# Kernel tuning notes

Hardware: AMD Instinct MI355X
Metric: run time of the kernel (lower is better)

Reference implementation:

```python
import jax, jax.numpy as jnp
import numpy as np

N, E, H, NF, EF = 50000, 400000, 128, 10, 10


def setup_inputs() -> dict:
    key = jax.random.key(0)
    ks = iter(jax.random.split(key, 24))
    rn = lambda shape, s=0.1: jax.random.normal(next(ks), shape, jnp.float32) * s
    z = lambda shape: jnp.zeros(shape, jnp.float32)
    o = lambda shape: jnp.ones(shape, jnp.float32)
    return {
        "x": jax.random.normal(next(ks), (N, NF), jnp.float32),
        "edge_index": jax.random.randint(next(ks), (2, E), 0, N, jnp.int32),
        "edge_attr": jax.random.normal(next(ks), (E, EF), jnp.float32),
        "ne_w": rn((NF, H)), "ne_b": z(H), "ne_g": o(H), "ne_beta": z(H),
        "ee_w": rn((EF, H)), "ee_b": z(H), "ee_g": o(H), "ee_beta": z(H),
        "gate_w": rn((3 * H, H)), "gate_b": z(H),
        "gatA_w": rn((2, H, H)), "gatA_asrc": rn((2, 8, 16)), "gatA_adst": rn((2, 8, 16)), "gatA_bias": z((2, H)),
        "gatB_w": rn((H, H)), "gatB_asrc": rn((1, H)), "gatB_adst": rn((1, H)), "gatB_bias": z(H),
        "ln_g": o((3, H)), "ln_b": z((3, H)),
        "c1_w": rn((2 * H, H)), "c1_b": z(H), "cl1_g": o(H), "cl1_b": z(H),
        "c2_w": rn((H, H // 2)), "c2_b": z(H // 2), "cl2_g": o(H // 2), "cl2_b": z(H // 2),
        "c3_w": rn((H // 2, 2)), "c3_b": z(2),
    }


def _ln(x, g, b):
    m = x.mean(-1, keepdims=True)
    v = ((x - m) ** 2).mean(-1, keepdims=True)
    return (x - m) / jnp.sqrt(v + 1e-5) * g + b


def _gat(h, src, dst, n, w, asrc, adst, bias, concat):
    # PyG GATConv: lin (no bias), per-edge leaky_relu score, segment softmax over dst, scatter-add
    heads, dout = asrc.shape
    xp = (h @ w).reshape(n, heads, dout)             # [N, heads, dout]
    a_s = (xp * asrc).sum(-1)                        # [N, heads]
    a_d = (xp * adst).sum(-1)
    e = jax.nn.leaky_relu(a_s[src] + a_d[dst], 0.2)  # [E2, heads]
    m = jax.ops.segment_max(e, dst, num_segments=n)
    ex = jnp.exp(e - m[dst])
    s = jax.ops.segment_sum(ex, dst, num_segments=n)
    alpha = ex / s[dst]                               # [E2, heads]
    out = jax.ops.segment_sum(xp[src] * alpha[..., None], dst, num_segments=n)  # [N, heads, dout]
    out = out.reshape(n, heads * dout) if concat else out.mean(1)
    return out + bias


def reference(x, edge_index, edge_attr, ne_w, ne_b, ne_g, ne_beta, ee_w, ee_b, ee_g, ee_beta,
              gate_w, gate_b, gatA_w, gatA_asrc, gatA_adst, gatA_bias, gatB_w, gatB_asrc,
              gatB_adst, gatB_bias, ln_g, ln_b, c1_w, c1_b, cl1_g, cl1_b, c2_w, c2_b,
              cl2_g, cl2_b, c3_w, c3_b):
    n = x.shape[0]
    row, col = edge_index[0], edge_index[1]
    loops = jnp.arange(n, dtype=edge_index.dtype)     # GATConv add_self_loops=True
    src_sl = jnp.concatenate([row, loops])
    dst_sl = jnp.concatenate([col, loops])

    h = jax.nn.relu(_ln(x @ ne_w + ne_b, ne_g, ne_beta))      # node encoder (dropout=eval)
    for l in range(2):
        h = _gat(h, src_sl, dst_sl, n, gatA_w[l], gatA_asrc[l], gatA_adst[l], gatA_bias[l], True)
        h = jax.nn.relu(_ln(h, ln_g[l], ln_b[l]))
    h = _gat(h, src_sl, dst_sl, n, gatB_w, gatB_asrc, gatB_adst, gatB_bias, False)
    h = jax.nn.relu(_ln(h, ln_g[2], ln_b[2]))

    s = h[row]
    d = h[col]
    e = jax.nn.relu(_ln(edge_attr @ ee_w + ee_b, ee_g, ee_beta))  # edge encoder
    gate = jax.nn.sigmoid(jnp.concatenate([s, d, e], axis=1) @ gate_w + gate_b)
    s = s + gate * e
    d = d + gate * e

    zc = jax.nn.relu(_ln(jnp.concatenate([s, d], axis=1) @ c1_w + c1_b, cl1_g, cl1_b))
    zc = jax.nn.relu(_ln(zc @ c2_w + c2_b, cl2_g, cl2_b))
    return zc @ c3_w + c3_b                                   # [E, num_classes]
```

## Files before the change

kernel.cpp:

```cpp
#include <hip/hip_runtime.h>
#include <hip/hip_bf16.h>

#define H 128
#define NFEAT 10
#define EFEAT 10
#define XPS 144

typedef __attribute__((ext_vector_type(8))) short bf16x8;
typedef __attribute__((ext_vector_type(4))) float f32x4;

__device__ __forceinline__ float bflo(unsigned v) { return __uint_as_float(v << 16); }
__device__ __forceinline__ float bfhi(unsigned v) { return __uint_as_float(v & 0xffff0000u); }
__device__ __forceinline__ unsigned bfpack(float a, float b) {
    __hip_bfloat16 h0 = __float2bfloat16(a), h1 = __float2bfloat16(b);
    return (unsigned)(*(unsigned short*)&h0) | ((unsigned)(*(unsigned short*)&h1) << 16);
}

__global__ __launch_bounds__(256) void k_degree(const int* __restrict__ col,
                                                int* __restrict__ deg, int E, int N) {
    int i = blockIdx.x * blockDim.x + threadIdx.x;
    int E2 = E + N;
    if (i < E2) {
        int d = (i < E) ? col[i] : (i - E);
        atomicAdd(&deg[d], 1);
    }
}

__global__ __launch_bounds__(1024) void k_scan(const int* __restrict__ deg,
                                               int* __restrict__ offs,
                                               int* __restrict__ cursor, int N) {
    __shared__ int ps[1024];
    int t = threadIdx.x;
    int chunk = (N + 1023) / 1024;
    int begin = t * chunk;
    int end = begin + chunk; if (end > N) end = N;
    int s = 0;
    for (int i = begin; i < end; i++) s += deg[i];
    if (begin >= N) s = 0;
    ps[t] = s;
    __syncthreads();
    for (int off = 1; off < 1024; off <<= 1) {
        int v = (t >= off) ? ps[t - off] : 0;
        __syncthreads();
        ps[t] += v;
        __syncthreads();
    }
    int run = (t == 0) ? 0 : ps[t - 1];
    if (begin < N) {
        for (int i = begin; i < end; i++) {
            offs[i] = run;
            cursor[i] = run;
            run += deg[i];
        }
    }
    if (t == 1023) offs[N] = ps[1023];
}

__global__ __launch_bounds__(256) void k_scatter(const int* __restrict__ rowp,
                                                 const int* __restrict__ colp,
                                                 int* __restrict__ cursor,
                                                 int* __restrict__ srcs, int E, int N) {
    int i = blockIdx.x * blockDim.x + threadIdx.x;
    if (i < E + N) {
        int s, d;
        if (i < E) { s = rowp[i]; d = colp[i]; }
        else       { s = i - E;  d = i - E; }
        int pos = atomicAdd(&cursor[d], 1);
        srcs[pos] = s;
    }
}

__global__ __launch_bounds__(256) void k_node_enc(const float* __restrict__ x,
                                                  const float* __restrict__ wm,
                                                  const float* __restrict__ b,
                                                  const float* __restrict__ g,
                                                  const float* __restrict__ beta,
                                                  __hip_bfloat16* __restrict__ h, int N) {
    int t = threadIdx.x;
    int w = t >> 6, l = t & 63;
    int n = blockIdx.x * 4 + w;
    if (n >= N) return;
    float xs[NFEAT];
#pragma unroll
    for (int k = 0; k < NFEAT; k++) xs[k] = x[(size_t)n * NFEAT + k];
    float a0 = b[2 * l], a1 = b[2 * l + 1];
#pragma unroll
    for (int k = 0; k < NFEAT; k++) {
        float2 wv = *(const float2*)&wm[k * H + 2 * l];
        a0 += xs[k] * wv.x;
        a1 += xs[k] * wv.y;
    }
    float p = a0 + a1;
#pragma unroll
    for (int s = 1; s < 64; s <<= 1) p += __shfl_xor(p, s, 64);
    float mean = p * (1.0f / H);
    float d0 = a0 - mean, d1 = a1 - mean;
    float q = d0 * d0 + d1 * d1;
#pragma unroll
    for (int s = 1; s < 64; s <<= 1) q += __shfl_xor(q, s, 64);
    float rstd = rsqrtf(q * (1.0f / H) + 1e-5f);
    float y0 = fmaxf(d0 * rstd * g[2 * l] + beta[2 * l], 0.0f);
    float y1 = fmaxf(d1 * rstd * g[2 * l + 1] + beta[2 * l + 1], 0.0f);
    *(unsigned*)&h[(size_t)n * H + 2 * l] = bfpack(y0, y1);
}

__global__ __launch_bounds__(256, 2) void k_gat_xp_mfma(
        const __hip_bfloat16* __restrict__ h_bf,
        const __hip_bfloat16* __restrict__ wT,
        const float* __restrict__ asrc,
        const float* __restrict__ adst,
        __hip_bfloat16* __restrict__ xp_bf,
        float* __restrict__ a_d,
        int heads, int N) {
    __shared__ __hip_bfloat16 Ws[128 * 136];
    __shared__ __hip_bfloat16 As[64 * 136];
    int t = threadIdx.x;
    int n0 = blockIdx.x * 64;

#pragma unroll
    for (int it = 0; it < 2; it++) {
        int idx = it * 256 + t;
        int row = idx >> 2, seg = idx & 3;
        const uint4* src = (const uint4*)(wT + row * 128 + seg * 32);
        uint4 v0 = src[0], v1 = src[1], v2 = src[2], v3 = src[3];
        uint4* dst = (uint4*)&Ws[row * 136 + seg * 32];
        dst[0] = v0; dst[1] = v1; dst[2] = v2; dst[3] = v3;
    }
    {
        int row = t >> 2, seg = t & 3;
        int n = n0 + row; if (n >= N) n = N - 1;
        const uint4* src = (const uint4*)(h_bf + (size_t)n * 128 + seg * 32);
        uint4 v0 = src[0], v1 = src[1], v2 = src[2], v3 = src[3];
        uint4* dst = (uint4*)&As[row * 136 + seg * 32];
        dst[0] = v0; dst[1] = v1; dst[2] = v2; dst[3] = v3;
    }
    __syncthreads();

    int w = t >> 6, l = t & 63, ln15 = l & 15, quad = l >> 4, q8 = quad * 8;
    f32x4 acc[8] = {};
#pragma unroll
    for (int k = 0; k < 128; k += 32) {
        bf16x8 af = *(const bf16x8*)&As[(w * 16 + ln15) * 136 + k + q8];
#pragma unroll
        for (int i = 0; i < 8; i++) {
            bf16x8 bfr = *(const bf16x8*)&Ws[(i * 16 + ln15) * 136 + k + q8];
            acc[i] = __builtin_amdgcn_mfma_f32_16x16x32_bf16(af, bfr, acc[i], 0, 0, 0);
        }
    }

    if (heads == 8) {
#pragma unroll
        for (int i = 0; i < 8; i++) {
            float av = asrc[i * 16 + ln15], dvv = adst[i * 16 + ln15];
            float ps[4], pd[4];
#pragma unroll
            for (int r = 0; r < 4; r++) { ps[r] = acc[i][r] * av; pd[r] = acc[i][r] * dvv; }
#pragma unroll
            for (int s = 1; s < 16; s <<= 1) {
#pragma unroll
                for (int r = 0; r < 4; r++) {
                    ps[r] += __shfl_xor(ps[r], s, 64);
                    pd[r] += __shfl_xor(pd[r], s, 64);
                }
            }
            if (ln15 == 0) {
#pragma unroll
                for (int r = 0; r < 4; r++) {
                    int n = n0 + w * 16 + quad * 4 + r;
                    if (n < N) {
                        *(float*)&xp_bf[(size_t)n * XPS + 128 + 2 * i] = ps[r];
                        a_d[(size_t)n * 8 + i] = pd[r];
                    }
                }
            }
        }
    } else {
        float ps[4] = {0, 0, 0, 0}, pd[4] = {0, 0, 0, 0};
#pragma unroll
        for (int i = 0; i < 8; i++) {
            float av = asrc[i * 16 + ln15], dvv = adst[i * 16 + ln15];
#pragma unroll
            for (int r = 0; r < 4; r++) { ps[r] += acc[i][r] * av; pd[r] += acc[i][r] * dvv; }
        }
#pragma unroll
        for (int s = 1; s < 16; s <<= 1) {
#pragma unroll
            for (int r = 0; r < 4; r++) {
                ps[r] += __shfl_xor(ps[r], s, 64);
                pd[r] += __shfl_xor(pd[r], s, 64);
            }
        }
        if (ln15 == 0) {
#pragma unroll
            for (int r = 0; r < 4; r++) {
                int n = n0 + w * 16 + quad * 4 + r;
                if (n < N) {
                    *(float*)&xp_bf[(size_t)n * XPS + 128] = ps[r];
                    a_d[n] = pd[r];
                }
            }
        }
    }

#pragma unroll
    for (int i = 0; i < 8; i++) {
#pragma unroll
        for (int r = 0; r < 4; r++) {
            int n = n0 + w * 16 + quad * 4 + r;
            if (n < N) xp_bf[(size_t)n * XPS + i * 16 + ln15] = __float2bfloat16(acc[i][r]);
        }
    }
}

__global__ __launch_bounds__(256) void k_gat_agg(const __hip_bfloat16* __restrict__ xp,
                                                 const float* __restrict__ a_d,
                                                 const int* __restrict__ offs,
                                                 const int* __restrict__ srcs,
                                                 const float* __restrict__ bias,
                                                 const float* __restrict__ g,
                                                 const float* __restrict__ b,
                                                 __hip_bfloat16* __restrict__ hout,
                                                 int heads, int N) {
    int t = threadIdx.x;
    int w = t >> 6, l = t & 63;
    int n = blockIdx.x * 4 + w;
    if (n >= N) return;
    int head = (heads == 8) ? (l >> 3) : 0;
    float adv = a_d[(size_t)n * heads + head];
    int s0 = offs[n], s1 = offs[n + 1];
    float acc0 = 0.0f, acc1 = 0.0f, den = 0.0f;
    int j = s0;
    for (; j + 4 <= s1; j += 4) {
        int s_[4];
#pragma unroll
        for (int u = 0; u < 4; u++) s_[u] = srcs[j + u];
        float e_[4]; unsigned v_[4];
#pragma unroll
        for (int u = 0; u < 4; u++) {
            const __hip_bfloat16* xr = xp + (size_t)s_[u] * XPS;
            e_[u] = ((const float*)xr)[64 + head];
            v_[u] = *(const unsigned*)&xr[2 * l];
        }
#pragma unroll
        for (int u = 0; u < 4; u++) {
            float e = e_[u] + adv;
            e = (e >= 0.0f) ? e : 0.2f * e;
            float ex = __expf(e);
            den += ex;
            acc0 += ex * bflo(v_[u]);
            acc1 += ex * bfhi(v_[u]);
        }
    }
    for (; j < s1; j++) {
        int s = srcs[j];
        const __hip_bfloat16* xr = xp + (size_t)s * XPS;
        float e = ((const float*)xr)[64 + head] + adv;
        e = (e >= 0.0f) ? e : 0.2f * e;
        float ex = __expf(e);
        den += ex;
        unsigned v = *(const unsigned*)&xr[2 * l];
        acc0 += ex * bflo(v);
        acc1 += ex * bfhi(v);
    }
    float inv = 1.0f / den;
    float v0 = acc0 * inv + bias[2 * l];
    float v1 = acc1 * inv + bias[2 * l + 1];
    float p = v0 + v1;
#pragma unroll
    for (int s = 1; s < 64; s <<= 1) p += __shfl_xor(p, s, 64);
    float mean = p * (1.0f / H);
    float d0 = v0 - mean, d1 = v1 - mean;
    float q = d0 * d0 + d1 * d1;
#pragma unroll
    for (int s = 1; s < 64; s <<= 1) q += __shfl_xor(q, s, 64);
    float rstd = rsqrtf(q * (1.0f / H) + 1e-5f);
    float y0 = fmaxf(d0 * rstd * g[2 * l] + b[2 * l], 0.0f);
    float y1 = fmaxf(d1 * rstd * g[2 * l + 1] + b[2 * l + 1], 0.0f);
    *(unsigned*)&hout[(size_t)n * H + 2 * l] = bfpack(y0, y1);
}

__global__ __launch_bounds__(256) void k_wprep(const float* __restrict__ gate_w,
                                               const float* __restrict__ c1_w,
                                               const float* __restrict__ c2_w,
                                               const float* __restrict__ gatA_w,
                                               const float* __restrict__ gatB_w,
                                               const float* __restrict__ ee_w,
                                               __hip_bfloat16* __restrict__ gate_sw,
                                               __hip_bfloat16* __restrict__ c1_sw,
                                               __hip_bfloat16* __restrict__ c2_sw,
                                               __hip_bfloat16* __restrict__ wT3,
                                               __hip_bfloat16* __restrict__ ee_sw) {
    int i = blockIdx.x * blockDim.x + threadIdx.x;
    if (i < 49152) {
        int j = i & 7, lane = (i >> 3) & 63, rest = i >> 9;
        int nt = rest & 7, kc = rest >> 3;
        int n = nt * 16 + (lane & 15);
        int k = kc * 32 + (lane >> 4) * 8 + j;
        gate_sw[i] = __float2bfloat16(gate_w[k * 128 + n]);
    } else if (i < 81920) {
        int m = i - 49152;
        int j = m & 7, lane = (m >> 3) & 63, rest = m >> 9;
        int nt = rest & 7, kc = rest >> 3;
        int n = nt * 16 + (lane & 15);
        int k = kc * 32 + (lane >> 4) * 8 + j;
        c1_sw[m] = __float2bfloat16(c1_w[k * 128 + n]);
    } else if (i < 90112) {
        int m = i - 81920;
        int j = m & 7, lane = (m >> 3) & 63, rest = m >> 9;
        int nt = rest & 3, kc = rest >> 2;
        int n = nt * 16 + (lane & 15);
        int k = kc * 32 + (lane >> 4) * 8 + j;
        c2_sw[m] = __float2bfloat16(c2_w[k * 64 + n]);
    } else if (i < 139264) {
        int m = i - 90112;
        int mat = m / 16384, r = m % 16384;
        int n = r / 128, k = r % 128;
        const float* src = (mat < 2) ? (gatA_w + (size_t)mat * 16384) : gatB_w;
        wT3[m] = __float2bfloat16(src[k * 128 + n]);
    } else if (i < 143360) {
        int m = i - 139264;
        int j = m & 7, lane = (m >> 3) & 63, nt = (m >> 9) & 7;
        int n = nt * 16 + (lane & 15);
        int k = (lane >> 4) * 8 + j;
        ee_sw[m] = (k < EFEAT) ? __float2bfloat16(ee_w[k * 128 + n]) : __float2bfloat16(0.0f);
    }
}

__global__ __launch_bounds__(256, 4) void k_edge_cls_mfma(
        const __hip_bfloat16* __restrict__ h_bf,
        const int* __restrict__ rowp, const int* __restrict__ colp,
        const float* __restrict__ eattr,
        const __hip_bfloat16* __restrict__ ee_sw, const float* __restrict__ ee_b,
        const float* __restrict__ ee_g, const float* __restrict__ ee_beta,
        const __hip_bfloat16* __restrict__ gate_sw, const float* __restrict__ gate_b,
        const __hip_bfloat16* __restrict__ c1_sw, const float* __restrict__ c1_b,
        const float* __restrict__ cl1_g, const float* __restrict__ cl1_b,
        const __hip_bfloat16* __restrict__ c2_sw, const float* __restrict__ c2_b,
        const float* __restrict__ cl2_g, const float* __restrict__ cl2_b,
        const float* __restrict__ c3_w, const float* __restrict__ c3_b,
        float* __restrict__ out, int E) {
    __shared__ __align__(16) __hip_bfloat16 Bs[4 * 16 * 264];
    int t = threadIdx.x;
    int w = t >> 6, l = t & 63;
    int ln15 = l & 15, quad = l >> 4, q8 = quad * 8;
    int e0 = blockIdx.x * 64;
    int rbase = w * 16;
    __hip_bfloat16* B = Bs + w * (16 * 264);

    int eF = e0 + rbase + ln15; if (eF >= E) eF = E - 1;
    const __hip_bfloat16* rowS = h_bf + (size_t)rowp[eF] * 128;
    const __hip_bfloat16* rowD = h_bf + (size_t)colp[eF] * 128;

    {
        bf16x8 afe;
#pragma unroll
        for (int j = 0; j < 8; j++) {
            int k = q8 + j;
            float v = (k < EFEAT) ? eattr[(size_t)eF * EFEAT + k] : 0.0f;
            __hip_bfloat16 hv = __float2bfloat16(v);
            afe[j] = *(short*)&hv;
        }
        f32x4 acc[8] = {};
#pragma unroll
        for (int i = 0; i < 8; i++) {
            bf16x8 bfr = *(const bf16x8*)(ee_sw + ((size_t)i * 64 + l) * 8);
            acc[i] = __builtin_amdgcn_mfma_f32_16x16x32_bf16(afe, bfr, acc[i], 0, 0, 0);
        }
#pragma unroll
        for (int i = 0; i < 8; i++) {
            float cb = ee_b[i * 16 + ln15];
#pragma unroll
            for (int r = 0; r < 4; r++) acc[i][r] += cb;
        }
        float mean[4], rstd[4];
#pragma unroll
        for (int r = 0; r < 4; r++) {
            float p = 0.0f;
#pragma unroll
            for (int i = 0; i < 8; i++) p += acc[i][r];
            p += __shfl_xor(p, 1, 64); p += __shfl_xor(p, 2, 64);
            p += __shfl_xor(p, 4, 64); p += __shfl_xor(p, 8, 64);
            mean[r] = p * (1.0f / 128.0f);
        }
#pragma unroll
        for (int r = 0; r < 4; r++) {
            float q = 0.0f;
#pragma unroll
            for (int i = 0; i < 8; i++) { float d = acc[i][r] - mean[r]; q += d * d; }
            q += __shfl_xor(q, 1, 64); q += __shfl_xor(q, 2, 64);
            q += __shfl_xor(q, 4, 64); q += __shfl_xor(q, 8, 64);
            rstd[r] = rsqrtf(q * (1.0f / 128.0f) + 1e-5f);
        }
#pragma unroll
        for (int i = 0; i < 8; i++) {
            int cn = i * 16 + ln15;
            float g1 = ee_g[cn], b1 = ee_beta[cn];
#pragma unroll
            for (int r = 0; r < 4; r++) {
                int qr = quad * 4 + r;
                float y = fmaxf((acc[i][r] - mean[r]) * rstd[r] * g1 + b1, 0.0f);
                B[qr * 264 + cn] = __float2bfloat16(y);
            }
        }
    }

    {
        f32x4 acc[8] = {};
        bf16x8 fifo[4];
#pragma unroll
        for (int s = 0; s < 4; s++)
            fifo[s] = *(const bf16x8*)(gate_sw + ((size_t)s * 64 + l) * 8);
        bf16x8 acur = *(const bf16x8*)(rowS + q8);
        bf16x8 anx;
#pragma unroll
        for (int s = 0; s < 96; s++) {
            int kc = s >> 3, i = s & 7;
            if (i == 0 && kc < 11) {
                int k1 = kc + 1;
                if (k1 < 4)      anx = *(const bf16x8*)(rowS + k1 * 32 + q8);
                else if (k1 < 8) anx = *(const bf16x8*)(rowD + (k1 - 4) * 32 + q8);
                else             anx = *(const bf16x8*)&B[ln15 * 264 + (k1 - 8) * 32 + q8];
            }
            bf16x8 bcur = fifo[s & 3];
            if (s + 4 < 96)
                fifo[s & 3] = *(const bf16x8*)(gate_sw + ((size_t)(s + 4) * 64 + l) * 8);
            acc[i] = __builtin_amdgcn_mfma_f32_16x16x32_bf16(acur, bcur, acc[i], 0, 0, 0);
            if (i == 7) acur = anx;
        }
#pragma unroll
        for (int r = 0; r < 4; r++) {
            int qr = quad * 4 + r;
            int er = e0 + rbase + qr; if (er >= E) er = E - 1;
            const __hip_bfloat16* rS = h_bf + (size_t)rowp[er] * 128;
            const __hip_bfloat16* rD = h_bf + (size_t)colp[er] * 128;
#pragma unroll
            for (int i = 0; i < 8; i++) {
                int cn = i * 16 + ln15;
                float gt = 1.0f / (1.0f + __expf(-(acc[i][r] + gate_b[cn])));
                float ef = __bfloat162float(B[qr * 264 + cn]);
                float s  = __bfloat162float(rS[cn]);
                float d  = __bfloat162float(rD[cn]);
                B[qr * 264 + cn]       = __float2bfloat16(s + gt * ef);
                B[qr * 264 + 128 + cn] = __float2bfloat16(d + gt * ef);
            }
        }
    }

    {
        f32x4 acc[8] = {};
        bf16x8 fifo[4];
#pragma unroll
        for (int s = 0; s < 4; s++)
            fifo[s] = *(const bf16x8*)(c1_sw + ((size_t)s * 64 + l) * 8);
        bf16x8 acur = *(const bf16x8*)&B[ln15 * 264 + q8];
        bf16x8 anx;
#pragma unroll
        for (int s = 0; s < 64; s++) {
            int kc = s >> 3, i = s & 7;
            if (i == 0 && kc < 7)
                anx = *(const bf16x8*)&B[ln15 * 264 + (kc + 1) * 32 + q8];
            bf16x8 bcur = fifo[s & 3];
            if (s + 4 < 64)
                fifo[s & 3] = *(const bf16x8*)(c1_sw + ((size_t)(s + 4) * 64 + l) * 8);
            acc[i] = __builtin_amdgcn_mfma_f32_16x16x32_bf16(acur, bcur, acc[i], 0, 0, 0);
            if (i == 7) acur = anx;
        }
#pragma unroll
        for (int i = 0; i < 8; i++) {
            float cb = c1_b[i * 16 + ln15];
#pragma unroll
            for (int r = 0; r < 4; r++) acc[i][r] += cb;
        }
        float mean[4], rstd[4];
#pragma unroll
        for (int r = 0; r < 4; r++) {
            float p = 0.0f;
#pragma unroll
            for (int i = 0; i < 8; i++) p += acc[i][r];
            p += __shfl_xor(p, 1, 64); p += __shfl_xor(p, 2, 64);
            p += __shfl_xor(p, 4, 64); p += __shfl_xor(p, 8, 64);
            mean[r] = p * (1.0f / 128.0f);
        }
#pragma unroll
        for (int r = 0; r < 4; r++) {
            float q = 0.0f;
#pragma unroll
            for (int i = 0; i < 8; i++) { float d = acc[i][r] - mean[r]; q += d * d; }
            q += __shfl_xor(q, 1, 64); q += __shfl_xor(q, 2, 64);
            q += __shfl_xor(q, 4, 64); q += __shfl_xor(q, 8, 64);
            rstd[r] = rsqrtf(q * (1.0f / 128.0f) + 1e-5f);
        }
#pragma unroll
        for (int i = 0; i < 8; i++) {
            int cn = i * 16 + ln15;
            float g1 = cl1_g[cn], b1 = cl1_b[cn];
#pragma unroll
            for (int r = 0; r < 4; r++) {
                int qr = quad * 4 + r;
                float y = fmaxf((acc[i][r] - mean[r]) * rstd[r] * g1 + b1, 0.0f);
                B[qr * 264 + cn] = __float2bfloat16(y);
            }
        }
    }

    {
        f32x4 acc[4] = {};
        bf16x8 fifo[4];
#pragma unroll
        for (int s = 0; s < 4; s++)
            fifo[s] = *(const bf16x8*)(c2_sw + ((size_t)s * 64 + l) * 8);
        bf16x8 acur = *(const bf16x8*)&B[ln15 * 264 + q8];
        bf16x8 anx;
#pragma unroll
        for (int s = 0; s < 16; s++) {
            int kc = s >> 2, i = s & 3;
            if (i == 0 && kc < 3)
                anx = *(const bf16x8*)&B[ln15 * 264 + (kc + 1) * 32 + q8];
            bf16x8 bcur = fifo[s & 3];
            if (s + 4 < 16)
                fifo[s & 3] = *(const bf16x8*)(c2_sw + ((size_t)(s + 4) * 64 + l) * 8);
            acc[i] = __builtin_amdgcn_mfma_f32_16x16x32_bf16(acur, bcur, acc[i], 0, 0, 0);
            if (i == 3) acur = anx;
        }
#pragma unroll
        for (int i = 0; i < 4; i++) {
            float cb = c2_b[i * 16 + ln15];
#pragma unroll
            for (int r = 0; r < 4; r++) acc[i][r] += cb;
        }
        float mean[4], rstd[4];
#pragma unroll
        for (int r = 0; r < 4; r++) {
            float p = 0.0f;
#pragma unroll
            for (int i = 0; i < 4; i++) p += acc[i][r];
            p += __shfl_xor(p, 1, 64); p += __shfl_xor(p, 2, 64);
            p += __shfl_xor(p, 4, 64); p += __shfl_xor(p, 8, 64);
            mean[r] = p * (1.0f / 64.0f);
        }
#pragma unroll
        for (int r = 0; r < 4; r++) {
            float q = 0.0f;
#pragma unroll
            for (int i = 0; i < 4; i++) { float d = acc[i][r] - mean[r]; q += d * d; }
            q += __shfl_xor(q, 1, 64); q += __shfl_xor(q, 2, 64);
            q += __shfl_xor(q, 4, 64); q += __shfl_xor(q, 8, 64);
            rstd[r] = rsqrtf(q * (1.0f / 64.0f) + 1e-5f);
        }
        float w0[4], w1[4];
#pragma unroll
        for (int i = 0; i < 4; i++) {
            float2 cw = *(const float2*)&c3_w[(i * 16 + ln15) * 2];
            w0[i] = cw.x; w1[i] = cw.y;
        }
#pragma unroll
        for (int r = 0; r < 4; r++) {
            float s0 = 0.0f, s1 = 0.0f;
#pragma unroll
            for (int i = 0; i < 4; i++) {
                int cn = i * 16 + ln15;
                float y = fmaxf((acc[i][r] - mean[r]) * rstd[r] * cl2_g[cn] + cl2_b[cn], 0.0f);
                s0 += y * w0[i];
                s1 += y * w1[i];
            }
            s0 += __shfl_xor(s0, 1, 64); s0 += __shfl_xor(s0, 2, 64);
            s0 += __shfl_xor(s0, 4, 64); s0 += __shfl_xor(s0, 8, 64);
            s1 += __shfl_xor(s1, 1, 64); s1 += __shfl_xor(s1, 2, 64);
            s1 += __shfl_xor(s1, 4, 64); s1 += __shfl_xor(s1, 8, 64);
            if (ln15 == 0) {
                int e = e0 + rbase + quad * 4 + r;
                if (e < E) {
                    float2 o; o.x = s0 + c3_b[0]; o.y = s1 + c3_b[1];
                    *(float2*)&out[(size_t)e * 2] = o;
                }
            }
        }
    }
}

extern "C" void kernel_launch(void* const* d_in, const int* in_sizes, int n_in,
                              void* d_out, int out_size, void* d_ws, size_t ws_size,
                              hipStream_t stream) {
    const float* x        = (const float*)d_in[0];
    const int*   eidx     = (const int*)d_in[1];
    const float* eattr    = (const float*)d_in[2];
    const float* ne_w     = (const float*)d_in[3];
    const float* ne_b     = (const float*)d_in[4];
    const float* ne_g     = (const float*)d_in[5];
    const float* ne_beta  = (const float*)d_in[6];
    const float* ee_w     = (const float*)d_in[7];
    const float* ee_b     = (const float*)d_in[8];
    const float* ee_g     = (const float*)d_in[9];
    const float* ee_beta  = (const float*)d_in[10];
    const float* gate_w   = (const float*)d_in[11];
    const float* gate_b   = (const float*)d_in[12];
    const float* gatA_w   = (const float*)d_in[13];
    const float* gatA_as  = (const float*)d_in[14];
    const float* gatA_ad  = (const float*)d_in[15];
    const float* gatA_bias= (const float*)d_in[16];
    const float* gatB_w   = (const float*)d_in[17];
    const float* gatB_as  = (const float*)d_in[18];
    const float* gatB_ad  = (const float*)d_in[19];
    const float* gatB_bias= (const float*)d_in[20];
    const float* ln_g     = (const float*)d_in[21];
    const float* ln_b     = (const float*)d_in[22];
    const float* c1_w     = (const float*)d_in[23];
    const float* c1_b     = (const float*)d_in[24];
    const float* cl1_g    = (const float*)d_in[25];
    const float* cl1_b    = (const float*)d_in[26];
    const float* c2_w     = (const float*)d_in[27];
    const float* c2_b     = (const float*)d_in[28];
    const float* cl2_g    = (const float*)d_in[29];
    const float* cl2_b    = (const float*)d_in[30];
    const float* c3_w     = (const float*)d_in[31];
    const float* c3_b     = (const float*)d_in[32];

    const int N = in_sizes[0] / NFEAT;
    const int E = in_sizes[1] / 2;
    const int E2 = E + N;
    const int* rowp = eidx;
    const int* colp = eidx + E;

    char* ws = (char*)d_ws;
    size_t off = 0;
    auto alloc = [&](size_t bytes) -> void* {
        void* p = ws + off;
        off = (off + bytes + 255) & ~(size_t)255;
        return p;
    };
    int*   deg    = (int*)alloc((size_t)N * 4);
    int*   cursor = (int*)alloc((size_t)N * 4);
    int*   offs   = (int*)alloc((size_t)(N + 1) * 4);
    int*   srcs   = (int*)alloc((size_t)E2 * 4);
    float* a_d    = (float*)alloc((size_t)N * 8 * 4);
    __hip_bfloat16* h_bfA  = (__hip_bfloat16*)alloc((size_t)N * H * 2);
    __hip_bfloat16* h_bfB  = (__hip_bfloat16*)alloc((size_t)N * H * 2);
    __hip_bfloat16* xp_bf  = (__hip_bfloat16*)alloc((size_t)N * XPS * 2);
    __hip_bfloat16* gate_sw= (__hip_bfloat16*)alloc((size_t)49152 * 2);
    __hip_bfloat16* c1_sw  = (__hip_bfloat16*)alloc((size_t)32768 * 2);
    __hip_bfloat16* c2_sw  = (__hip_bfloat16*)alloc((size_t)8192 * 2);
    __hip_bfloat16* wT3    = (__hip_bfloat16*)alloc((size_t)3 * 128 * 128 * 2);
    __hip_bfloat16* ee_sw  = (__hip_bfloat16*)alloc((size_t)4096 * 2);
    (void)ws_size;

    k_wprep<<<(143360 + 255) / 256, 256, 0, stream>>>(gate_w, c1_w, c2_w, gatA_w, gatB_w, ee_w,
                                                      gate_sw, c1_sw, c2_sw, wT3, ee_sw);

    hipMemsetAsync(deg, 0, (size_t)N * 4, stream);
    k_degree<<<(E2 + 255) / 256, 256, 0, stream>>>(colp, deg, E, N);
    k_scan<<<1, 1024, 0, stream>>>(deg, offs, cursor, N);
    k_scatter<<<(E2 + 255) / 256, 256, 0, stream>>>(rowp, colp, cursor, srcs, E, N);

    int ngrid = (N + 3) / 4;
    k_node_enc<<<ngrid, 256, 0, stream>>>(x, ne_w, ne_b, ne_g, ne_beta, h_bfA, N);

    int xpgrid = (N + 63) / 64;
    __hip_bfloat16* hin = h_bfA;
    __hip_bfloat16* hout = h_bfB;
    for (int l = 0; l < 2; l++) {
        k_gat_xp_mfma<<<xpgrid, 256, 0, stream>>>(hin, wT3 + (size_t)l * 16384,
                                                  gatA_as + l * H, gatA_ad + l * H,
                                                  xp_bf, a_d, 8, N);
        k_gat_agg<<<ngrid, 256, 0, stream>>>(xp_bf, a_d, offs, srcs,
                                             gatA_bias + l * H, ln_g + l * H, ln_b + l * H,
                                             hout, 8, N);
        __hip_bfloat16* tmp = hin; hin = hout; hout = tmp;
    }
    k_gat_xp_mfma<<<xpgrid, 256, 0, stream>>>(hin, wT3 + (size_t)2 * 16384,
                                              gatB_as, gatB_ad,
                                              xp_bf, a_d, 1, N);
    k_gat_agg<<<ngrid, 256, 0, stream>>>(xp_bf, a_d, offs, srcs,
                                         gatB_bias, ln_g + 2 * H, ln_b + 2 * H,
                                         hout, 1, N);

    k_edge_cls_mfma<<<(E + 63) / 64, 256, 0, stream>>>(
        hout, rowp, colp, eattr,
        ee_sw, ee_b, ee_g, ee_beta,
        gate_sw, gate_b,
        c1_sw, c1_b, cl1_g, cl1_b,
        c2_sw, c2_b, cl2_g, cl2_b,
        c3_w, c3_b,
        (float*)d_out, E);
}
```

Measured before the change: 681.9 us.

## Process two edge tiles per wave and stage only gated edge term in LDS

Each wave of the edge classifier now handles 32 edges as two 16-row MFMA tiles, so every weight fragment loaded from global memory feeds two MFMAs. The LDS buffer shrinks to hold only the encoded edge features and then gate*e; the s+gate*e and d+gate*e inputs to c1 are rebuilt on the fly by re-reading the gathered node rows and adding in bf16, instead of being materialized in shared memory. The launch-bounds occupancy hint is dropped because the doubled accumulators raise register pressure, and the grid is halved. The risks are lower occupancy and extra global gather traffic for the recomputed node rows.

```diff
diff --git a/kernel.cpp b/kernel.cpp
--- a/kernel.cpp
+++ b/kernel.cpp
@@ -14,6 +14,17 @@
 __device__ __forceinline__ unsigned bfpack(float a, float b) {
     __hip_bfloat16 h0 = __float2bfloat16(a), h1 = __float2bfloat16(b);
     return (unsigned)(*(unsigned short*)&h0) | ((unsigned)(*(unsigned short*)&h1) << 16);
+}
+__device__ __forceinline__ bf16x8 bfadd8(bf16x8 a, bf16x8 b) {
+    bf16x8 r;
+#pragma unroll
+    for (int j = 0; j < 8; j++) {
+        float fa = __uint_as_float(((unsigned)(unsigned short)a[j]) << 16);
+        float fb = __uint_as_float(((unsigned)(unsigned short)b[j]) << 16);
+        __hip_bfloat16 h = __float2bfloat16(fa + fb);
+        r[j] = *(short*)&h;
+    }
+    return r;
 }
 
 __global__ __launch_bounds__(256) void k_degree(const int* __restrict__ col,
@@ -326,7 +337,7 @@
     }
 }
 
-__global__ __launch_bounds__(256, 4) void k_edge_cls_mfma(
+__global__ __launch_bounds__(256) void k_edge_cls_mfma(
         const __hip_bfloat16* __restrict__ h_bf,
         const int* __restrict__ rowp, const int* __restrict__ colp,
         const float* __restrict__ eattr,
@@ -339,213 +350,207 @@
         const float* __restrict__ cl2_g, const float* __restrict__ cl2_b,
         const float* __restrict__ c3_w, const float* __restrict__ c3_b,
         float* __restrict__ out, int E) {
-    __shared__ __align__(16) __hip_bfloat16 Bs[4 * 16 * 264];
+    __shared__ __align__(16) __hip_bfloat16 Gs[4 * 32 * 136];
     int t = threadIdx.x;
     int w = t >> 6, l = t & 63;
     int ln15 = l & 15, quad = l >> 4, q8 = quad * 8;
-    int e0 = blockIdx.x * 64;
-    int rbase = w * 16;
-    __hip_bfloat16* B = Bs + w * (16 * 264);
-
-    int eF = e0 + rbase + ln15; if (eF >= E) eF = E - 1;
-    const __hip_bfloat16* rowS = h_bf + (size_t)rowp[eF] * 128;
-    const __hip_bfloat16* rowD = h_bf + (size_t)colp[eF] * 128;
+    int ebase = blockIdx.x * 128 + w * 32;
+    __hip_bfloat16* G = Gs + w * (32 * 136);
+
+    const __hip_bfloat16* rowS[2];
+    const __hip_bfloat16* rowD[2];
+    int eAf[2];
+#pragma unroll
+    for (int mt = 0; mt < 2; mt++) {
+        int e = ebase + mt * 16 + ln15; if (e >= E) e = E - 1;
+        eAf[mt] = e;
+        rowS[mt] = h_bf + (size_t)rowp[e] * 128;
+        rowD[mt] = h_bf + (size_t)colp[e] * 128;
+    }
 
     {
-        bf16x8 afe;
+        bf16x8 afe[2];
+#pragma unroll
+        for (int mt = 0; mt < 2; mt++)
 #pragma unroll
         for (int j = 0; j < 8; j++) {
             int k = q8 + j;
-            float v = (k < EFEAT) ? eattr[(size_t)eF * EFEAT + k] : 0.0f;
+            float v = (k < EFEAT) ? eattr[(size_t)eAf[mt] * EFEAT + k] : 0.0f;
             __hip_bfloat16 hv = __float2bfloat16(v);
-            afe[j] = *(short*)&hv;
-        }
-        f32x4 acc[8] = {};
+            afe[mt][j] = *(short*)&hv;
+        }
+        f32x4 acc[2][8] = {};
 #pragma unroll
         for (int i = 0; i < 8; i++) {
             bf16x8 bfr = *(const bf16x8*)(ee_sw + ((size_t)i * 64 + l) * 8);
-            acc[i] = __builtin_amdgcn_mfma_f32_16x16x32_bf16(afe, bfr, acc[i], 0, 0, 0);
-        }
-#pragma unroll
-        for (int i = 0; i < 8; i++) {
-            float cb = ee_b[i * 16 + ln15];
-#pragma unroll
-            for (int r = 0; r < 4; r++) acc[i][r] += cb;
-        }
-        float mean[4], rstd[4];
-#pragma unroll
-        for (int r = 0; r < 4; r++) {
-            float p = 0.0f;
-#pragma unroll
-            for (int i = 0; i < 8; i++) p += acc[i][r];
-            p += __shfl_xor(p, 1, 64); p += __shfl_xor(p, 2, 64);
-            p += __shfl_xor(p, 4, 64); p += __shfl_xor(p, 8, 64);
-            mean[r] = p * (1.0f / 128.0f);
-        }
-#pragma unroll
-        for (int r = 0; r < 4; r++) {
-            float q = 0.0f;
-#pragma unroll
-            for (int i = 0; i < 8; i++) { float d = acc[i][r] - mean[r]; q += d * d; }
-            q += __shfl_xor(q, 1, 64); q += __shfl_xor(q, 2, 64);
-            q += __shfl_xor(q, 4, 64); q += __shfl_xor(q, 8, 64);
-            rstd[r] = rsqrtf(q * (1.0f / 128.0f) + 1e-5f);
-        }
-#pragma unroll
-        for (int i = 0; i < 8; i++) {
-            int cn = i * 16 + ln15;
-            float g1 = ee_g[cn], b1 = ee_beta[cn];
+            acc[0][i] = __builtin_amdgcn_mfma_f32_16x16x32_bf16(afe[0], bfr, acc[0][i], 0, 0, 0);
+            acc[1][i] = __builtin_amdgcn_mfma_f32_16x16x32_bf16(afe[1], bfr, acc[1][i], 0, 0, 0);
+        }
+#pragma unroll
+        for (int mt = 0; mt < 2; mt++) {
 #pragma unroll
             for (int r = 0; r < 4; r++) {
-                int qr = quad * 4 + r;
-                float y = fmaxf((acc[i][r] - mean[r]) * rstd[r] * g1 + b1, 0.0f);
-                B[qr * 264 + cn] = __float2bfloat16(y);
+                float p = 0.0f;
+#pragma unroll
+                for (int i = 0; i < 8; i++) p += acc[mt][i][r] + ee_b[i * 16 + ln15];
+                p += __shfl_xor(p, 1, 64); p += __shfl_xor(p, 2, 64);
+                p += __shfl_xor(p, 4, 64); p += __shfl_xor(p, 8, 64);
+                float mean = p * (1.0f / 128.0f);
+                float q = 0.0f;
+#pragma unroll
+                for (int i = 0; i < 8; i++) {
+                    float d = acc[mt][i][r] + ee_b[i * 16 + ln15] - mean;
+                    q += d * d;
+                }
+                q += __shfl_xor(q, 1, 64); q += __shfl_xor(q, 2, 64);
+                q += __shfl_xor(q, 4, 64); q += __shfl_xor(q, 8, 64);
+                float rstd = rsqrtf(q * (1.0f / 128.0f) + 1e-5f);
+                int row = mt * 16 + quad * 4 + r;
+#pragma unroll
+                for (int i = 0; i < 8; i++) {
+                    int cn = i * 16 + ln15;
+                    float z = acc[mt][i][r] + ee_b[cn];
+                    float y = fmaxf((z - mean) * rstd * ee_g[cn] + ee_beta[cn], 0.0f);
+                    G[row * 136 + cn] = __float2bfloat16(y);
+                }
             }
         }
     }
 
     {
-        f32x4 acc[8] = {};
+        f32x4 acc[2][8] = {};
         bf16x8 fifo[4];
 #pragma unroll
         for (int s = 0; s < 4; s++)
             fifo[s] = *(const bf16x8*)(gate_sw + ((size_t)s * 64 + l) * 8);
-        bf16x8 acur = *(const bf16x8*)(rowS + q8);
-        bf16x8 anx;
+        bf16x8 a0 = *(const bf16x8*)(rowS[0] + q8);
+        bf16x8 a1 = *(const bf16x8*)(rowS[1] + q8);
+        bf16x8 a0n, a1n;
 #pragma unroll
         for (int s = 0; s < 96; s++) {
             int kc = s >> 3, i = s & 7;
             if (i == 0 && kc < 11) {
                 int k1 = kc + 1;
-                if (k1 < 4)      anx = *(const bf16x8*)(rowS + k1 * 32 + q8);
-                else if (k1 < 8) anx = *(const bf16x8*)(rowD + (k1 - 4) * 32 + q8);
-                else             anx = *(const bf16x8*)&B[ln15 * 264 + (k1 - 8) * 32 + q8];
+                if (k1 < 4) {
+                    a0n = *(const bf16x8*)(rowS[0] + k1 * 32 + q8);
+                    a1n = *(const bf16x8*)(rowS[1] + k1 * 32 + q8);
+                } else if (k1 < 8) {
+                    a0n = *(const bf16x8*)(rowD[0] + (k1 - 4) * 32 + q8);
+                    a1n = *(const bf16x8*)(rowD[1] + (k1 - 4) * 32 + q8);
+                } else {
+                    a0n = *(const bf16x8*)&G[ln15 * 136 + (k1 - 8) * 32 + q8];
+                    a1n = *(const bf16x8*)&G[(16 + ln15) * 136 + (k1 - 8) * 32 + q8];
+                }
             }
             bf16x8 bcur = fifo[s & 3];
             if (s + 4 < 96)
                 fifo[s & 3] = *(const bf16x8*)(gate_sw + ((size_t)(s + 4) * 64 + l) * 8);
-            acc[i] = __builtin_amdgcn_mfma_f32_16x16x32_bf16(acur, bcur, acc[i], 0, 0, 0);
-            if (i == 7) acur = anx;
-        }
+            acc[0][i] = __builtin_amdgcn_mfma_f32_16x16x32_bf16(a0, bcur, acc[0][i], 0, 0, 0);
+            acc[1][i] = __builtin_amdgcn_mfma_f32_16x16x32_bf16(a1, bcur, acc[1][i], 0, 0, 0);
+            if (i == 7) { a0 = a0n; a1 = a1n; }
+        }
+#pragma unroll
+        for (int mt = 0; mt < 2; mt++)
 #pragma unroll
         for (int r = 0; r < 4; r++) {
-            int qr = quad * 4 + r;
-            int er = e0 + rbase + qr; if (er >= E) er = E - 1;
-            const __hip_bfloat16* rS = h_bf + (size_t)rowp[er] * 128;
-            const __hip_bfloat16* rD = h_bf + (size_t)colp[er] * 128;
+            int row = mt * 16 + quad * 4 + r;
 #pragma unroll
             for (int i = 0; i < 8; i++) {
                 int cn = i * 16 + ln15;
-                float gt = 1.0f / (1.0f + __expf(-(acc[i][r] + gate_b[cn])));
-                float ef = __bfloat162float(B[qr * 264 + cn]);
-                float s  = __bfloat162float(rS[cn]);
-                float d  = __bfloat162float(rD[cn]);
-                B[qr * 264 + cn]       = __float2bfloat16(s + gt * ef);
-                B[qr * 264 + 128 + cn] = __float2bfloat16(d + gt * ef);
+                float gt = 1.0f / (1.0f + __expf(-(acc[mt][i][r] + gate_b[cn])));
+                float ef = __bfloat162float(G[row * 136 + cn]);
+                G[row * 136 + cn] = __float2bfloat16(gt * ef);
             }
         }
     }
 
     {
-        f32x4 acc[8] = {};
+        f32x4 acc[2][8] = {};
         bf16x8 fifo[4];
 #pragma unroll
         for (int s = 0; s < 4; s++)
             fifo[s] = *(const bf16x8*)(c1_sw + ((size_t)s * 64 + l) * 8);
-        bf16x8 acur = *(const bf16x8*)&B[ln15 * 264 + q8];
-        bf16x8 anx;
+        bf16x8 a0, a1;
+        {
+            bf16x8 s0 = *(const bf16x8*)(rowS[0] + q8);
+            bf16x8 s1 = *(const bf16x8*)(rowS[1] + q8);
+            bf16x8 g0 = *(const bf16x8*)&G[ln15 * 136 + q8];
+            bf16x8 g1 = *(const bf16x8*)&G[(16 + ln15) * 136 + q8];
+            a0 = bfadd8(s0, g0); a1 = bfadd8(s1, g1);
+        }
+        bf16x8 a0n, a1n;
 #pragma unroll
         for (int s = 0; s < 64; s++) {
             int kc = s >> 3, i = s & 7;
-            if (i == 0 && kc < 7)
-                anx = *(const bf16x8*)&B[ln15 * 264 + (kc + 1) * 32 + q8];
+            if (i == 0 && kc < 7) {
+                int k1 = kc + 1, kq = k1 & 3;
+                const __hip_bfloat16* p0 = (k1 < 4) ? rowS[0] : rowD[0];
+                const __hip_bfloat16* p1 = (k1 < 4) ? rowS[1] : rowD[1];
+                bf16x8 s0 = *(const bf16x8*)(p0 + kq * 32 + q8);
+                bf16x8 s1 = *(const bf16x8*)(p1 + kq * 32 + q8);
+                bf16x8 g0 = *(const bf16x8*)&G[ln15 * 136 + kq * 32 + q8];
+                bf16x8 g1 = *(const bf16x8*)&G[(16 + ln15) * 136 + kq * 32 + q8];
+                a0n = bfadd8(s0, g0); a1n = bfadd8(s1, g1);
+            }
             bf16x8 bcur = fifo[s & 3];
             if (s + 4 < 64)
                 fifo[s & 3] = *(const bf16x8*)(c1_sw + ((size_t)(s + 4) * 64 + l) * 8);
-            acc[i] = __builtin_amdgcn_mfma_f32_16x16x32_bf16(acur, bcur, acc[i], 0, 0, 0);
-            if (i == 7) acur = anx;
-        }
-#pragma unroll
-        for (int i = 0; i < 8; i++) {
-            float cb = c1_b[i * 16 + ln15];
-#pragma unroll
-            for (int r = 0; r < 4; r++) acc[i][r] += cb;
-        }
-        float mean[4], rstd[4];
+            acc[0][i] = __builtin_amdgcn_mfma_f32_16x16x32_bf16(a0, bcur, acc[0][i], 0, 0, 0);
+            acc[1][i] = __builtin_amdgcn_mfma_f32_16x16x32_bf16(a1, bcur, acc[1][i], 0, 0, 0);
+            if (i == 7) { a0 = a0n; a1 = a1n; }
+        }
+#pragma unroll
+        for (int mt = 0; mt < 2; mt++)
 #pragma unroll
         for (int r = 0; r < 4; r++) {
             float p = 0.0f;
 #pragma unroll
-            for (int i = 0; i < 8; i++) p += acc[i][r];
+            for (int i = 0; i < 8; i++) p += acc[mt][i][r] + c1_b[i * 16 + ln15];
             p += __shfl_xor(p, 1, 64); p += __shfl_xor(p, 2, 64);
             p += __shfl_xor(p, 4, 64); p += __shfl_xor(p, 8, 64);
-            mean[r] = p * (1.0f / 128.0f);
-        }
-#pragma unroll
-        for (int r = 0; r < 4; r++) {
+            float mean = p * (1.0f / 128.0f);
             float q = 0.0f;
 #pragma unroll
-            for (int i = 0; i < 8; i++) { float d = acc[i][r] - mean[r]; q += d * d; }
+            for (int i = 0; i < 8; i++) {
+                float d = acc[mt][i][r] + c1_b[i * 16 + ln15] - mean;
+                q += d * d;
+            }
             q += __shfl_xor(q, 1, 64); q += __shfl_xor(q, 2, 64);
             q += __shfl_xor(q, 4, 64); q += __shfl_xor(q, 8, 64);
-            rstd[r] = rsqrtf(q * (1.0f / 128.0f) + 1e-5f);
-        }
-#pragma unroll
-        for (int i = 0; i < 8; i++) {
-            int cn = i * 16 + ln15;
-            float g1 = cl1_g[cn], b1 = cl1_b[cn];
-#pragma unroll
-            for (int r = 0; r < 4; r++) {
-                int qr = quad * 4 + r;
-                float y = fmaxf((acc[i][r] - mean[r]) * rstd[r] * g1 + b1, 0.0f);
-                B[qr * 264 + cn] = __float2bfloat16(y);
+            float rstd = rsqrtf(q * (1.0f / 128.0f) + 1e-5f);
+            int row = mt * 16 + quad * 4 + r;
+#pragma unroll
+            for (int i = 0; i < 8; i++) {
+                int cn = i * 16 + ln15;
+                float z = acc[mt][i][r] + c1_b[cn];
+                float y = fmaxf((z - mean) * rstd * cl1_g[cn] + cl1_b[cn], 0.0f);
+                G[row * 136 + cn] = __float2bfloat16(y);
             }
         }
     }
 
     {
-        f32x4 acc[4] = {};
+        f32x4 acc[2][4] = {};
         bf16x8 fifo[4];
 #pragma unroll
         for (int s = 0; s < 4; s++)
             fifo[s] = *(const bf16x8*)(c2_sw + ((size_t)s * 64 + l) * 8);
-        bf16x8 acur = *(const bf16x8*)&B[ln15 * 264 + q8];
-        bf16x8 anx;
+        bf16x8 a0 = *(const bf16x8*)&G[ln15 * 136 + q8];
+        bf16x8 a1 = *(const bf16x8*)&G[(16 + ln15) * 136 + q8];
+        bf16x8 a0n, a1n;
 #pragma unroll
         for (int s = 0; s < 16; s++) {
             int kc = s >> 2, i = s & 3;
-            if (i == 0 && kc < 3)
-                anx = *(const bf16x8*)&B[ln15 * 264 + (kc + 1) * 32 + q8];
+            if (i == 0 && kc < 3) {
+                a0n = *(const bf16x8*)&G[ln15 * 136 + (kc + 1) * 32 + q8];
+                a1n = *(const bf16x8*)&G[(16 + ln15) * 136 + (kc + 1) * 32 + q8];
+            }
             bf16x8 bcur = fifo[s & 3];
             if (s + 4 < 16)
                 fifo[s & 3] = *(const bf16x8*)(c2_sw + ((size_t)(s + 4) * 64 + l) * 8);
-            acc[i] = __builtin_amdgcn_mfma_f32_16x16x32_bf16(acur, bcur, acc[i], 0, 0, 0);
-            if (i == 3) acur = anx;
-        }
-#pragma unroll
-        for (int i = 0; i < 4; i++) {
-            float cb = c2_b[i * 16 + ln15];
-#pragma unroll
-            for (int r = 0; r < 4; r++) acc[i][r] += cb;
-        }
-        float mean[4], rstd[4];
-#pragma unroll
-        for (int r = 0; r < 4; r++) {
-            float p = 0.0f;
-#pragma unroll
-            for (int i = 0; i < 4; i++) p += acc[i][r];
-            p += __shfl_xor(p, 1, 64); p += __shfl_xor(p, 2, 64);
-            p += __shfl_xor(p, 4, 64); p += __shfl_xor(p, 8, 64);
-            mean[r] = p * (1.0f / 64.0f);
-        }
-#pragma unroll
-        for (int r = 0; r < 4; r++) {
-            float q = 0.0f;
-#pragma unroll
-            for (int i = 0; i < 4; i++) { float d = acc[i][r] - mean[r]; q += d * d; }
-            q += __shfl_xor(q, 1, 64); q += __shfl_xor(q, 2, 64);
-            q += __shfl_xor(q, 4, 64); q += __shfl_xor(q, 8, 64);
-            rstd[r] = rsqrtf(q * (1.0f / 64.0f) + 1e-5f);
+            acc[0][i] = __builtin_amdgcn_mfma_f32_16x16x32_bf16(a0, bcur, acc[0][i], 0, 0, 0);
+            acc[1][i] = __builtin_amdgcn_mfma_f32_16x16x32_bf16(a1, bcur, acc[1][i], 0, 0, 0);
+            if (i == 3) { a0 = a0n; a1 = a1n; }
         }
         float w0[4], w1[4];
 #pragma unroll
@@ -554,12 +559,30 @@
             w0[i] = cw.x; w1[i] = cw.y;
         }
 #pragma unroll
+        for (int mt = 0; mt < 2; mt++)
+#pragma unroll
         for (int r = 0; r < 4; r++) {
+            float p = 0.0f;
+#pragma unroll
+            for (int i = 0; i < 4; i++) p += acc[mt][i][r] + c2_b[i * 16 + ln15];
+            p += __shfl_xor(p, 1, 64); p += __shfl_xor(p, 2, 64);
+            p += __shfl_xor(p, 4, 64); p += __shfl_xor(p, 8, 64);
+            float mean = p * (1.0f / 64.0f);
+            float q = 0.0f;
+#pragma unroll
+            for (int i = 0; i < 4; i++) {
+                float d = acc[mt][i][r] + c2_b[i * 16 + ln15] - mean;
+                q += d * d;
+            }
+            q += __shfl_xor(q, 1, 64); q += __shfl_xor(q, 2, 64);
+            q += __shfl_xor(q, 4, 64); q += __shfl_xor(q, 8, 64);
+            float rstd = rsqrtf(q * (1.0f / 64.0f) + 1e-5f);
             float s0 = 0.0f, s1 = 0.0f;
 #pragma unroll
             for (int i = 0; i < 4; i++) {
                 int cn = i * 16 + ln15;
-                float y = fmaxf((acc[i][r] - mean[r]) * rstd[r] * cl2_g[cn] + cl2_b[cn], 0.0f);
+                float z = acc[mt][i][r] + c2_b[cn];
+                float y = fmaxf((z - mean) * rstd * cl2_g[cn] + cl2_b[cn], 0.0f);
                 s0 += y * w0[i];
                 s1 += y * w1[i];
             }
@@ -568,7 +591,7 @@
             s1 += __shfl_xor(s1, 1, 64); s1 += __shfl_xor(s1, 2, 64);
             s1 += __shfl_xor(s1, 4, 64); s1 += __shfl_xor(s1, 8, 64);
             if (ln15 == 0) {
-                int e = e0 + rbase + quad * 4 + r;
+                int e = ebase + mt * 16 + quad * 4 + r;
                 if (e < E) {
                     float2 o; o.x = s0 + c3_b[0]; o.y = s1 + c3_b[1];
                     *(float2*)&out[(size_t)e * 2] = o;
@@ -673,7 +696,7 @@
                                          gatB_bias, ln_g + 2 * H, ln_b + 2 * H,
                                          hout, 1, N);
 
-    k_edge_cls_mfma<<<(E + 63) / 64, 256, 0, stream>>>(
+    k_edge_cls_mfma<<<(E + 127) / 128, 256, 0, stream>>>(
         hout, rowp, colp, eattr,
         ee_sw, ee_b, ee_g, ee_beta,
         gate_sw, gate_b,
```

Measured after the change: 850.8 us. +24.8%, slower.
